# Kernel tuning notes

Measured on AMD Instinct MI355X. Metric: run time of the kernel, lower is better.

Reference implementation:

```python
import jax, jax.numpy as jnp
import numpy as np

L, D, H, V, T_BLK, B, T = 6, 768, 12, 32000, 1024, 4, 1024
HD = D // H          # head size = 64
FF = 4 * D           # FFN hidden
EPS = 1e-5


def _ln(x, g, b):
    m = x.mean(-1, keepdims=True)
    v = ((x - m) ** 2).mean(-1, keepdims=True)
    return (x - m) * jax.lax.rsqrt(v + EPS) * g + b


def _attn(q_in, kv_in, wqkv, wo, bo, causal):
    # wqkv: [3, D, D]; heads batched (equivalent to concat of per-head Linear outputs)
    Bq, Tq, _ = q_in.shape
    Tk = kv_in.shape[1]
    q = (q_in @ wqkv[0]).reshape(Bq, Tq, H, HD)
    k = (kv_in @ wqkv[1]).reshape(Bq, Tk, H, HD)
    v = (kv_in @ wqkv[2]).reshape(Bq, Tk, H, HD)
    wei = jnp.einsum('bqhd,bkhd->bhqk', q, k) * (HD ** -0.5)
    if causal:
        mask = jnp.tril(jnp.ones((Tq, Tk), dtype=bool))
        wei = jnp.where(mask, wei, -jnp.inf)
    wei = jax.nn.softmax(wei, axis=-1)
    out = jnp.einsum('bhqk,bkhd->bqhd', wei, v).reshape(Bq, Tq, D)
    return out @ wo + bo


def _ffn(x, w1, b1, w2, b2):
    return jax.nn.relu(x @ w1 + b1) @ w2 + b2


def _forward(idx, encoder_input,
             enc_tok, enc_pos, enc_qkv, enc_wo, enc_bo, enc_w1, enc_b1, enc_w2, enc_b2,
             enc_ln1g, enc_ln1b, enc_ln2g, enc_ln2b, enc_lnfg, enc_lnfb,
             dec_tok, dec_pos, dec_qkv, dec_wo, dec_bo, dec_cqkv, dec_cwo, dec_cbo,
             dec_w1, dec_b1, dec_w2, dec_b2,
             dec_ln1g, dec_ln1b, dec_ln2g, dec_ln2b, dec_ln3g, dec_ln3b,
             dec_lnfg, dec_lnfb, lm_w, lm_b):
    # ---- encoder (NOTE: original Head always applies causal tril, so encoder is causal) ----
    Te = encoder_input.shape[1]
    x = enc_tok[encoder_input] + enc_pos[:Te]
    for i in range(L):
        h = _ln(x, enc_ln1g[i], enc_ln1b[i])
        x = x + _attn(h, h, enc_qkv[i], enc_wo[i], enc_bo[i], causal=True)
        h = _ln(x, enc_ln2g[i], enc_ln2b[i])
        x = x + _ffn(h, enc_w1[i], enc_b1[i], enc_w2[i], enc_b2[i])
    enc_out = _ln(x, enc_lnfg, enc_lnfb)
    # ---- decoder ----
    Td = idx.shape[1]
    y = dec_tok[idx] + dec_pos[:Td]
    for i in range(L):
        h = _ln(y, dec_ln1g[i], dec_ln1b[i])
        y = y + _attn(h, h, dec_qkv[i], dec_wo[i], dec_bo[i], causal=True)
        h = _ln(y, dec_ln2g[i], dec_ln2b[i])
        y = y + _attn(h, enc_out, dec_cqkv[i], dec_cwo[i], dec_cbo[i], causal=False)
        h = _ln(y, dec_ln3g[i], dec_ln3b[i])
        y = y + _ffn(h, dec_w1[i], dec_b1[i], dec_w2[i], dec_b2[i])
    y = _ln(y, dec_lnfg, dec_lnfb)
    return y @ lm_w + lm_b  # logits [B, T, V]


def setup_inputs() -> dict:
    key = jax.random.key(0)
    keys = iter(jax.random.split(key, 80))
    def nrm(shape, s=0.02):
        return jax.random.normal(next(keys), shape, dtype=jnp.float32) * s
    z = lambda shape: jnp.zeros(shape, jnp.float32)
    o = lambda shape: jnp.ones(shape, jnp.float32)
    inp = {}
    inp['idx'] = jax.random.randint(next(keys), (B, T), 0, V)
    inp['encoder_input'] = jax.random.randint(next(keys), (B, T), 0, V)
    # encoder params
    inp['enc_tok'] = nrm((V, D)); inp['enc_pos'] = nrm((T_BLK, D))
    inp['enc_qkv'] = nrm((L, 3, D, D)); inp['enc_wo'] = nrm((L, D, D)); inp['enc_bo'] = z((L, D))
    inp['enc_w1'] = nrm((L, D, FF)); inp['enc_b1'] = z((L, FF))
    inp['enc_w2'] = nrm((L, FF, D)); inp['enc_b2'] = z((L, D))
    inp['enc_ln1g'] = o((L, D)); inp['enc_ln1b'] = z((L, D))
    inp['enc_ln2g'] = o((L, D)); inp['enc_ln2b'] = z((L, D))
    inp['enc_lnfg'] = o((D,)); inp['enc_lnfb'] = z((D,))
    # decoder params
    inp['dec_tok'] = nrm((V, D)); inp['dec_pos'] = nrm((T_BLK, D))
    inp['dec_qkv'] = nrm((L, 3, D, D)); inp['dec_wo'] = nrm((L, D, D)); inp['dec_bo'] = z((L, D))
    inp['dec_cqkv'] = nrm((L, 3, D, D)); inp['dec_cwo'] = nrm((L, D, D)); inp['dec_cbo'] = z((L, D))
    inp['dec_w1'] = nrm((L, D, FF)); inp['dec_b1'] = z((L, FF))
    inp['dec_w2'] = nrm((L, FF, D)); inp['dec_b2'] = z((L, D))
    inp['dec_ln1g'] = o((L, D)); inp['dec_ln1b'] = z((L, D))
    inp['dec_ln2g'] = o((L, D)); inp['dec_ln2b'] = z((L, D))
    inp['dec_ln3g'] = o((L, D)); inp['dec_ln3b'] = z((L, D))
    inp['dec_lnfg'] = o((D,)); inp['dec_lnfb'] = z((D,))
    inp['lm_w'] = nrm((D, V)); inp['lm_b'] = z((V,))
    return inp


def reference(idx, encoder_input,
              enc_tok, enc_pos, enc_qkv, enc_wo, enc_bo, enc_w1, enc_b1, enc_w2, enc_b2,
              enc_ln1g, enc_ln1b, enc_ln2g, enc_ln2b, enc_lnfg, enc_lnfb,
              dec_tok, dec_pos, dec_qkv, dec_wo, dec_bo, dec_cqkv, dec_cwo, dec_cbo,
              dec_w1, dec_b1, dec_w2, dec_b2,
              dec_ln1g, dec_ln1b, dec_ln2g, dec_ln2b, dec_ln3g, dec_ln3b,
              dec_lnfg, dec_lnfb, lm_w, lm_b):
    return _forward(idx, encoder_input,
                    enc_tok, enc_pos, enc_qkv, enc_wo, enc_bo, enc_w1, enc_b1, enc_w2, enc_b2,
                    enc_ln1g, enc_ln1b, enc_ln2g, enc_ln2b, enc_lnfg, enc_lnfb,
                    dec_tok, dec_pos, dec_qkv, dec_wo, dec_bo, dec_cqkv, dec_cwo, dec_cbo,
                    dec_w1, dec_b1, dec_w2, dec_b2,
                    dec_ln1g, dec_ln1b, dec_ln2g, dec_ln2b, dec_ln3g, dec_ln3b,
                    dec_lnfg, dec_lnfb, lm_w, lm_b)
```

## Files before the change

### kernel.cpp

```cpp
#include <hip/hip_runtime.h>


typedef __bf16 bf16x8 __attribute__((ext_vector_type(8)));
typedef float  f32x4  __attribute__((ext_vector_type(4)));
typedef unsigned short u16x4 __attribute__((ext_vector_type(4)));
typedef unsigned short u16x8 __attribute__((ext_vector_type(8)));

constexpr int Lc = 6, Dc = 768, Hc = 12, HDc = 64, Vc = 32000;
constexpr int Bc = 4, Tc = 1024, FFc = 3072;
constexpr int Mtot = Bc * Tc;

static __device__ __forceinline__ unsigned short f2bf(float f) {
  union { float f; unsigned u; } x; x.f = f;
  unsigned r = x.u + 0x7fffu + ((x.u >> 16) & 1u);
  return (unsigned short)(r >> 16);
}
static __device__ __forceinline__ float bf2f(unsigned short s) {
  union { unsigned u; float f; } c; c.u = (unsigned)s << 16; return c.f;
}

static __device__ __forceinline__ void gl_lds16(const unsigned short* g, unsigned short* l) {
  __builtin_amdgcn_global_load_lds(
      (const __attribute__((address_space(1))) unsigned int*)g,
      (__attribute__((address_space(3))) unsigned int*)l, 16, 0, 0);
}

static __device__ __forceinline__ float blockReduceSum(float v, float* red) {
  #pragma unroll
  for (int o = 32; o; o >>= 1) v += __shfl_xor(v, o, 64);
  int w = threadIdx.x >> 6;
  __syncthreads();
  if ((threadIdx.x & 63) == 0) red[w] = v;
  __syncthreads();
  return red[0] + red[1] + red[2] + red[3];
}

__global__ __launch_bounds__(256) void wconv_k(const float* __restrict__ W,
                                               unsigned short* __restrict__ WT,
                                               int K, int N) {
  __shared__ float t[32][33];
  const long zoff = (long)blockIdx.z * K * N;
  const int k0 = blockIdx.x * 32, n0 = blockIdx.y * 32;
  const int tid = threadIdx.x;
  const int rr = tid >> 3;
  const int cc = (tid & 7) * 4;
  f32x4 v = *reinterpret_cast<const f32x4*>(W + zoff + (long)(k0 + rr) * N + n0 + cc);
  #pragma unroll
  for (int j = 0; j < 4; j++) t[rr][cc + j] = v[j];
  __syncthreads();
  u16x4 o;
  #pragma unroll
  for (int j = 0; j < 4; j++) o[j] = f2bf(t[cc + j][rr]);
  *reinterpret_cast<u16x4*>(WT + zoff + (long)(n0 + rr) * K + k0 + cc) = o;
}

__global__ __launch_bounds__(256) void vtrans_k(const unsigned short* __restrict__ V,
                                                unsigned short* __restrict__ VT) {
  __shared__ unsigned short t[64][65];
  const int bh = blockIdx.y;
  const int b = bh / Hc, h = bh % Hc;
  const int t0 = blockIdx.x * 64;
  const int tid = threadIdx.x;
  const int rr = tid >> 3;
  const int c8 = (tid & 7) * 8;
  #pragma unroll
  for (int rep = 0; rep < 2; rep++) {
    int row = rep * 32 + rr;
    u16x8 v = *reinterpret_cast<const u16x8*>(V + (long)(b * Tc + t0 + row) * Dc + h * HDc + c8);
    #pragma unroll
    for (int j = 0; j < 8; j++) t[row][c8 + j] = v[j];
  }
  __syncthreads();
  #pragma unroll
  for (int rep = 0; rep < 2; rep++) {
    int hd = rep * 32 + rr;
    u16x8 o;
    #pragma unroll
    for (int j = 0; j < 8; j++) o[j] = t[c8 + j][hd];
    *reinterpret_cast<u16x8*>(VT + ((long)bh * HDc + hd) * Tc + t0 + c8) = o;
  }
}

__global__ __launch_bounds__(256) void embed_k(const int* __restrict__ idx,
                                               const float* __restrict__ tok,
                                               const float* __restrict__ pos,
                                               float* __restrict__ out) {
  const long row = blockIdx.x;
  const int t = (int)(row % Tc);
  const long id = idx[row];
  #pragma unroll
  for (int j = 0; j < 3; j++) {
    int e = threadIdx.x + j * 256;
    out[row * Dc + e] = tok[id * Dc + e] + pos[(long)t * Dc + e];
  }
}

__global__ __launch_bounds__(256) void ln_k(const float* __restrict__ X,
                                            const float* __restrict__ g,
                                            const float* __restrict__ bta,
                                            unsigned short* __restrict__ out) {
  __shared__ float red[4];
  const long row = blockIdx.x;
  const int tid = threadIdx.x;
  float v[3];
  #pragma unroll
  for (int j = 0; j < 3; j++) v[j] = X[row * Dc + tid + j * 256];
  float s = v[0] + v[1] + v[2];
  s = blockReduceSum(s, red);
  float mean = s * (1.f / 768.f);
  float q = 0.f;
  #pragma unroll
  for (int j = 0; j < 3; j++) { float d = v[j] - mean; q += d * d; }
  q = blockReduceSum(q, red);
  float rstd = rsqrtf(q * (1.f / 768.f) + 1e-5f);
  #pragma unroll
  for (int j = 0; j < 3; j++) {
    int e = tid + j * 256;
    out[row * Dc + e] = f2bf((v[j] - mean) * rstd * g[e] + bta[e]);
  }
}

template <bool CAUSAL>
__global__ __launch_bounds__(256) void flash_k(
    const unsigned short* __restrict__ Q,
    const unsigned short* __restrict__ K,
    const unsigned short* __restrict__ VT,
    unsigned short* __restrict__ O) {
  __shared__ __align__(16) unsigned short Ks[128 * 64];
  __shared__ __align__(16) unsigned short Vs[64 * 128];
  __shared__ __align__(16) unsigned short Ps[4][32 * 128];

  const int tid = threadIdx.x;
  const int lane = tid & 63;
  const int w = tid >> 6;
  const int lane16 = lane & 15;
  const int l4 = lane >> 4;
  const int bh = blockIdx.y;
  const int b = bh / Hc, h = bh % Hc;
  const int q0 = blockIdx.x * 128;

  const unsigned short* Qb = Q + ((long)b * Tc) * Dc + h * HDc;
  const unsigned short* Kb = K + ((long)b * Tc) * Dc + h * HDc;
  const unsigned short* Vb = VT + (long)bh * HDc * Tc;
  unsigned short* Ob = O + ((long)b * Tc) * Dc + h * HDc;

  bf16x8 qf[2][2];
  #pragma unroll
  for (int m = 0; m < 2; m++)
    #pragma unroll
    for (int kk = 0; kk < 2; kk++) {
      u16x8 raw = *reinterpret_cast<const u16x8*>(
          Qb + (long)(q0 + w * 32 + m * 16 + lane16) * Dc + kk * 32 + l4 * 8);
      bf16x8 f;
      #pragma unroll
      for (int j = 0; j < 8; j++) f[j] = (__bf16)(bf2f(raw[j]) * 0.125f);
      qf[m][kk] = f;
    }

  float mrow[2][4], lrow[2][4];
  f32x4 accO[2][4];
  #pragma unroll
  for (int m = 0; m < 2; m++)
    #pragma unroll
    for (int r = 0; r < 4; r++) { mrow[m][r] = -1e30f; lrow[m][r] = 0.f; }
  #pragma unroll
  for (int m = 0; m < 2; m++)
    #pragma unroll
    for (int d4 = 0; d4 < 4; d4++)
      #pragma unroll
      for (int r = 0; r < 4; r++) accO[m][d4][r] = 0.f;

  const int nch = CAUSAL ? (blockIdx.x + 1) : (Tc / 128);
  for (int c = 0; c < nch; c++) {
    const int k0 = c * 128;
    __syncthreads();
    #pragma unroll
    for (int it = 0; it < 4; it++) {
      int u = (it * 4 + w) * 64 + lane;
      int r = u >> 3, s = u & 7;
      gl_lds16(Kb + (long)(k0 + r) * Dc + ((s ^ (r & 7)) * 8), &Ks[(it * 4 + w) * 512]);
      int r2 = u >> 4, s2 = u & 15;
      gl_lds16(Vb + (long)r2 * Tc + k0 + ((s2 ^ (r2 & 7)) * 8), &Vs[(it * 4 + w) * 512]);
    }
    __syncthreads();

    f32x4 sacc[2][8];
    #pragma unroll
    for (int m = 0; m < 2; m++)
      #pragma unroll
      for (int n = 0; n < 8; n++)
        #pragma unroll
        for (int r = 0; r < 4; r++) sacc[m][n][r] = 0.f;
    #pragma unroll
    for (int n = 0; n < 8; n++) {
      int row = n * 16 + lane16;
      #pragma unroll
      for (int kk = 0; kk < 2; kk++) {
        bf16x8 kf = *reinterpret_cast<const bf16x8*>(
            &Ks[row * 64 + (((kk * 4 + l4) ^ (row & 7)) * 8)]);
        sacc[0][n] = __builtin_amdgcn_mfma_f32_16x16x32_bf16(qf[0][kk], kf, sacc[0][n], 0, 0, 0);
        sacc[1][n] = __builtin_amdgcn_mfma_f32_16x16x32_bf16(qf[1][kk], kf, sacc[1][n], 0, 0, 0);
      }
    }

    if (CAUSAL && c == nch - 1) {
      #pragma unroll
      for (int m = 0; m < 2; m++)
        #pragma unroll
        for (int n = 0; n < 8; n++)
          #pragma unroll
          for (int r = 0; r < 4; r++) {
            int kcol = k0 + n * 16 + lane16;
            int q = q0 + w * 32 + m * 16 + l4 * 4 + r;
            if (kcol > q) sacc[m][n][r] = -1e30f;
          }
    }

    #pragma unroll
    for (int m = 0; m < 2; m++)
      #pragma unroll
      for (int r = 0; r < 4; r++) {
        float smax = sacc[m][0][r];
        #pragma unroll
        for (int n = 1; n < 8; n++) smax = fmaxf(smax, sacc[m][n][r]);
        #pragma unroll
        for (int off = 1; off < 16; off <<= 1) smax = fmaxf(smax, __shfl_xor(smax, off, 64));
        float mold = mrow[m][r];
        float mnew = fmaxf(mold, smax);
        float sc = __expf(mold - mnew);
        float psum = 0.f;
        unsigned short pv[8];
        #pragma unroll
        for (int n = 0; n < 8; n++) {
          float p = __expf(sacc[m][n][r] - mnew);
          psum += p;
          pv[n] = f2bf(p);
        }
        #pragma unroll
        for (int off = 1; off < 16; off <<= 1) psum += __shfl_xor(psum, off, 64);
        lrow[m][r] = lrow[m][r] * sc + psum;
        mrow[m][r] = mnew;
        #pragma unroll
        for (int d4 = 0; d4 < 4; d4++) accO[m][d4][r] *= sc;
        int prow = m * 16 + l4 * 4 + r;
        #pragma unroll
        for (int n = 0; n < 8; n++) {
          int col = n * 16 + lane16;
          Ps[w][prow * 128 + (((col >> 3) ^ (prow & 7)) * 8) + (col & 7)] = pv[n];
        }
      }

    #pragma unroll
    for (int kk = 0; kk < 4; kk++) {
      bf16x8 pa[2];
      #pragma unroll
      for (int m = 0; m < 2; m++) {
        int arow = m * 16 + lane16;
        pa[m] = *reinterpret_cast<const bf16x8*>(
            &Ps[w][arow * 128 + (((kk * 4 + l4) ^ (arow & 7)) * 8)]);
      }
      #pragma unroll
      for (int d4 = 0; d4 < 4; d4++) {
        int vrow = d4 * 16 + lane16;
        bf16x8 vf = *reinterpret_cast<const bf16x8*>(
            &Vs[vrow * 128 + (((kk * 4 + l4) ^ (vrow & 7)) * 8)]);
        accO[0][d4] = __builtin_amdgcn_mfma_f32_16x16x32_bf16(pa[0], vf, accO[0][d4], 0, 0, 0);
        accO[1][d4] = __builtin_amdgcn_mfma_f32_16x16x32_bf16(pa[1], vf, accO[1][d4], 0, 0, 0);
      }
    }
  }

  #pragma unroll
  for (int m = 0; m < 2; m++)
    #pragma unroll
    for (int r = 0; r < 4; r++) {
      float inv = 1.f / lrow[m][r];
      int q = q0 + w * 32 + m * 16 + l4 * 4 + r;
      #pragma unroll
      for (int d4 = 0; d4 < 4; d4++)
        Ob[(long)q * Dc + d4 * 16 + lane16] = f2bf(accO[m][d4][r] * inv);
    }
}

template <int BM, int BN, int MF, int NF, bool HASBIAS, bool RELU, bool HASRES, bool OUTBF>
__global__ __launch_bounds__(256) void gemm_k(
    const unsigned short* __restrict__ A, long sAb, long sAh, int lda,
    const unsigned short* __restrict__ BT, long sBb, long sBh, int ldb,
    void* Cp, long sCb, long sCh, int ldc,
    const float* __restrict__ bias,
    const float* __restrict__ Res, int ldr,
    int K, int nH, float alpha) {
  constexpr int BK = 64;
  __shared__ __align__(16) unsigned short As[2][BM * BK];
  __shared__ __align__(16) unsigned short Bs[2][BN * BK];

  const int tid = threadIdx.x;
  const int lane = tid & 63;
  const int w = tid >> 6;
  const int wr = w >> 1, wc = w & 1;
  const int lane16 = lane & 15;
  const int l4 = lane >> 4;

  const int z = blockIdx.z;
  const int bb = z / nH, hh = z % nH;
  const long offA = sAb * bb + sAh * hh;
  const long offB = sBb * bb + sBh * hh;
  const long offC = sCb * bb + sCh * hh;

  const int m0 = blockIdx.x * BM;
  const int n0 = blockIdx.y * BN;

  const int sr = lane >> 3;
  const int sgl = ((lane & 7) ^ sr) * 8;

  const unsigned short* Ab = A + offA + (long)m0 * lda;
  const unsigned short* Bb = BT + offB + (long)n0 * ldb;

  const unsigned short* aP[BM / 32];
  #pragma unroll
  for (int j = 0; j < BM / 32; j++)
    aP[j] = Ab + (long)(w * (BM / 4) + j * 8 + sr) * lda + sgl;
  const unsigned short* bP[BN / 32];
  #pragma unroll
  for (int j = 0; j < BN / 32; j++)
    bP[j] = Bb + (long)(w * (BN / 4) + j * 8 + sr) * ldb + sgl;

  f32x4 acc[MF][NF];
  #pragma unroll
  for (int m = 0; m < MF; m++)
    #pragma unroll
    for (int n = 0; n < NF; n++)
      #pragma unroll
      for (int r = 0; r < 4; r++) acc[m][n][r] = 0.f;

  auto STAGE = [&](int buf, int k0) {
    #pragma unroll
    for (int j = 0; j < BM / 32; j++)
      gl_lds16(aP[j] + k0, &As[buf][(w * (BM / 4) + j * 8) * BK]);
    #pragma unroll
    for (int j = 0; j < BN / 32; j++)
      gl_lds16(bP[j] + k0, &Bs[buf][(w * (BN / 4) + j * 8) * BK]);
  };
  auto COMPUTE = [&](int buf) {
    #pragma unroll
    for (int kk = 0; kk < 2; kk++) {
      bf16x8 af[MF], bfr[NF];
      #pragma unroll
      for (int m = 0; m < MF; m++) {
        int row = wr * MF * 16 + m * 16 + lane16;
        af[m] = *reinterpret_cast<const bf16x8*>(
            &As[buf][row * BK + (((kk * 4 + l4) ^ (lane16 & 7)) * 8)]);
      }
      #pragma unroll
      for (int n = 0; n < NF; n++) {
        int row = wc * NF * 16 + n * 16 + lane16;
        bfr[n] = *reinterpret_cast<const bf16x8*>(
            &Bs[buf][row * BK + (((kk * 4 + l4) ^ (lane16 & 7)) * 8)]);
      }
      #pragma unroll
      for (int m = 0; m < MF; m++)
        #pragma unroll
        for (int n = 0; n < NF; n++)
          acc[m][n] = __builtin_amdgcn_mfma_f32_16x16x32_bf16(af[m], bfr[n], acc[m][n], 0, 0, 0);
    }
  };

  const int nt = K / BK;
  int cur = 0;
  STAGE(0, 0);
  __syncthreads();
  for (int t = 0; t < nt; t++) {
    if (t + 1 < nt) STAGE(cur ^ 1, (t + 1) * BK);
    COMPUTE(cur);
    __syncthreads();
    cur ^= 1;
  }

  const int r0 = m0 + wr * MF * 16;
  const int c0 = n0 + wc * NF * 16;
  #pragma unroll
  for (int m = 0; m < MF; m++) {
    #pragma unroll
    for (int n = 0; n < NF; n++) {
      #pragma unroll
      for (int r = 0; r < 4; r++) {
        int rr = r0 + m * 16 + l4 * 4 + r;
        int cc = c0 + n * 16 + lane16;
        float v = acc[m][n][r] * alpha;
        if constexpr (HASBIAS) v += bias[cc];
        if constexpr (RELU) v = fmaxf(v, 0.f);
        if constexpr (HASRES) v += Res[offC + (long)rr * ldr + cc];
        if constexpr (OUTBF) ((unsigned short*)Cp)[offC + (long)rr * ldc + cc] = f2bf(v);
        else                 ((float*)Cp)[offC + (long)rr * ldc + cc] = v;
      }
    }
  }
}

extern "C" void kernel_launch(void* const* d_in, const int* in_sizes, int n_in,
                              void* d_out, int out_size, void* d_ws, size_t ws_size,
                              hipStream_t stream) {
  (void)in_sizes; (void)n_in; (void)out_size;

  const int*   idx      = (const int*)d_in[0];
  const int*   enc_in   = (const int*)d_in[1];
  const float* enc_tok  = (const float*)d_in[2];
  const float* enc_pos  = (const float*)d_in[3];
  const float* enc_qkv  = (const float*)d_in[4];
  const float* enc_wo   = (const float*)d_in[5];
  const float* enc_bo   = (const float*)d_in[6];
  const float* enc_w1   = (const float*)d_in[7];
  const float* enc_b1   = (const float*)d_in[8];
  const float* enc_w2   = (const float*)d_in[9];
  const float* enc_b2   = (const float*)d_in[10];
  const float* enc_ln1g = (const float*)d_in[11];
  const float* enc_ln1b = (const float*)d_in[12];
  const float* enc_ln2g = (const float*)d_in[13];
  const float* enc_ln2b = (const float*)d_in[14];
  const float* enc_lnfg = (const float*)d_in[15];
  const float* enc_lnfb = (const float*)d_in[16];
  const float* dec_tok  = (const float*)d_in[17];
  const float* dec_pos  = (const float*)d_in[18];
  const float* dec_qkv  = (const float*)d_in[19];
  const float* dec_wo   = (const float*)d_in[20];
  const float* dec_bo   = (const float*)d_in[21];
  const float* dec_cqkv = (const float*)d_in[22];
  const float* dec_cwo  = (const float*)d_in[23];
  const float* dec_cbo  = (const float*)d_in[24];
  const float* dec_w1   = (const float*)d_in[25];
  const float* dec_b1   = (const float*)d_in[26];
  const float* dec_w2   = (const float*)d_in[27];
  const float* dec_b2   = (const float*)d_in[28];
  const float* dec_ln1g = (const float*)d_in[29];
  const float* dec_ln1b = (const float*)d_in[30];
  const float* dec_ln2g = (const float*)d_in[31];
  const float* dec_ln2b = (const float*)d_in[32];
  const float* dec_ln3g = (const float*)d_in[33];
  const float* dec_ln3b = (const float*)d_in[34];
  const float* dec_lnfg = (const float*)d_in[35];
  const float* dec_lnfb = (const float*)d_in[36];
  const float* lm_w     = (const float*)d_in[37];
  const float* lm_b     = (const float*)d_in[38];

  constexpr long De2 = (long)Dc * Dc;
  constexpr long DF  = (long)Dc * FFc;

  unsigned short* wcache = (unsigned short*)d_out;
  size_t woff = 0;
  auto take = [&](size_t n) { unsigned short* p = wcache + woff; woff += n; return p; };
  unsigned short* enc_qkvT  = take(18ul * De2);
  unsigned short* enc_woT   = take(6ul * De2);
  unsigned short* enc_w1T   = take(6ul * DF);
  unsigned short* enc_w2T   = take(6ul * DF);
  unsigned short* dec_qkvT  = take(18ul * De2);
  unsigned short* dec_woT   = take(6ul * De2);
  unsigned short* dec_cqkvT = take(18ul * De2);
  unsigned short* dec_cwoT  = take(6ul * De2);
  unsigned short* dec_w1T   = take(6ul * DF);
  unsigned short* dec_w2T   = take(6ul * DF);

  char* ws = (char*)d_ws;
  const size_t need = (size_t)Dc * Vc * 2 + 2ull * Mtot * Dc * 4 + 3ull * Mtot * Dc * 2 +
                      3ull * Mtot * Dc * 2 + (size_t)Mtot * FFc * 2 + (size_t)Mtot * Dc * 2 +
                      (size_t)Bc * Hc * HDc * Tc * 2 + 4096;
  if (ws_size < need) return;
  auto takeW = [&](size_t bytes) { char* p = ws; ws += (bytes + 255) & ~255ull; return p; };
  unsigned short* lm_wT = (unsigned short*)takeW((size_t)Dc * Vc * 2);
  float* xe             = (float*)takeW((size_t)Mtot * Dc * 4);
  float* xd             = (float*)takeW((size_t)Mtot * Dc * 4);
  unsigned short* hbf   = (unsigned short*)takeW((size_t)Mtot * Dc * 2);
  unsigned short* qkvb  = (unsigned short*)takeW(3ull * Mtot * Dc * 2);
  unsigned short* ao    = (unsigned short*)takeW((size_t)Mtot * Dc * 2);
  unsigned short* mid   = (unsigned short*)takeW((size_t)Mtot * FFc * 2);
  unsigned short* eo    = (unsigned short*)takeW((size_t)Mtot * Dc * 2);
  unsigned short* vT    = (unsigned short*)takeW((size_t)Bc * Hc * HDc * Tc * 2);
  unsigned short* qb = qkvb;
  unsigned short* kb = qkvb + (size_t)Mtot * Dc;
  unsigned short* vb = qkvb + 2ull * Mtot * Dc;

  const dim3 TB(256);

  wconv_k<<<dim3(Dc/32, Dc/32, 18), TB, 0, stream>>>(enc_qkv, enc_qkvT, Dc, Dc);
  wconv_k<<<dim3(Dc/32, Dc/32,  6), TB, 0, stream>>>(enc_wo,  enc_woT,  Dc, Dc);
  wconv_k<<<dim3(Dc/32, FFc/32, 6), TB, 0, stream>>>(enc_w1,  enc_w1T,  Dc, FFc);
  wconv_k<<<dim3(FFc/32, Dc/32, 6), TB, 0, stream>>>(enc_w2,  enc_w2T,  FFc, Dc);
  wconv_k<<<dim3(Dc/32, Dc/32, 18), TB, 0, stream>>>(dec_qkv, dec_qkvT, Dc, Dc);
  wconv_k<<<dim3(Dc/32, Dc/32,  6), TB, 0, stream>>>(dec_wo,  dec_woT,  Dc, Dc);
  wconv_k<<<dim3(Dc/32, Dc/32, 18), TB, 0, stream>>>(dec_cqkv,dec_cqkvT,Dc, Dc);
  wconv_k<<<dim3(Dc/32, Dc/32,  6), TB, 0, stream>>>(dec_cwo, dec_cwoT, Dc, Dc);
  wconv_k<<<dim3(Dc/32, FFc/32, 6), TB, 0, stream>>>(dec_w1,  dec_w1T,  Dc, FFc);
  wconv_k<<<dim3(FFc/32, Dc/32, 6), TB, 0, stream>>>(dec_w2,  dec_w2T,  FFc, Dc);
  wconv_k<<<dim3(Dc/32, Vc/32,  1), TB, 0, stream>>>(lm_w,    lm_wT,    Dc, Vc);

  auto LN = [&](const float* X, const float* g, const float* b, unsigned short* o) {
    ln_k<<<dim3(Mtot), TB, 0, stream>>>(X, g, b, o);
  };
  auto QKV3 = [&](const unsigned short* Abf, const unsigned short* W3T) {
    gemm_k<128,64,4,2,false,false,false,true><<<dim3(Mtot/128, Dc/64, 3), TB, 0, stream>>>(
        Abf, 0, 0, Dc, W3T, De2, 0, Dc,
        qkvb, (long)Mtot*Dc, 0, Dc, nullptr, nullptr, 0, Dc, 1, 1.f);
  };
  auto PROJ1 = [&](const unsigned short* Abf, const unsigned short* WT, unsigned short* Cb) {
    gemm_k<128,64,4,2,false,false,false,true><<<dim3(Mtot/128, Dc/64, 1), TB, 0, stream>>>(
        Abf, 0, 0, Dc, WT, 0, 0, Dc,
        Cb, 0, 0, Dc, nullptr, nullptr, 0, Dc, 1, 1.f);
  };
  auto KV2 = [&](const unsigned short* Abf, const unsigned short* W2T) {
    gemm_k<128,64,4,2,false,false,false,true><<<dim3(Mtot/128, Dc/64, 2), TB, 0, stream>>>(
        Abf, 0, 0, Dc, W2T, De2, 0, Dc,
        kb, (long)Mtot*Dc, 0, Dc, nullptr, nullptr, 0, Dc, 1, 1.f);
  };
  auto VT = [&]() {
    vtrans_k<<<dim3(Tc/64, Bc*Hc), TB, 0, stream>>>(vb, vT);
  };
  auto FLASH = [&](bool causal) {
    if (causal) flash_k<true ><<<dim3(Tc/128, Bc*Hc), TB, 0, stream>>>(qb, kb, vT, ao);
    else        flash_k<false><<<dim3(Tc/128, Bc*Hc), TB, 0, stream>>>(qb, kb, vT, ao);
  };
  auto ORES = [&](const unsigned short* Abf, const unsigned short* WT, const float* bias, float* X) {
    gemm_k<128,64,4,2,true,false,true,false><<<dim3(Mtot/128, Dc/64, 1), TB, 0, stream>>>(
        Abf, 0, 0, Dc, WT, 0, 0, Dc,
        X, 0, 0, Dc, bias, X, Dc, Dc, 1, 1.f);
  };
  auto FFN1 = [&](const unsigned short* Abf, const unsigned short* WT, const float* bias) {
    gemm_k<128,128,4,4,true,true,false,true><<<dim3(Mtot/128, FFc/128, 1), TB, 0, stream>>>(
        Abf, 0, 0, Dc, WT, 0, 0, Dc,
        mid, 0, 0, FFc, bias, nullptr, 0, Dc, 1, 1.f);
  };
  auto FFN2 = [&](const unsigned short* WT, const float* bias, float* X) {
    gemm_k<128,64,4,2,true,false,true,false><<<dim3(Mtot/128, Dc/64, 1), TB, 0, stream>>>(
        mid, 0, 0, FFc, WT, 0, 0, FFc,
        X, 0, 0, Dc, bias, X, Dc, FFc, 1, 1.f);
  };

  embed_k<<<dim3(Mtot), TB, 0, stream>>>(enc_in, enc_tok, enc_pos, xe);
  for (int i = 0; i < Lc; i++) {
    LN(xe, enc_ln1g + i * Dc, enc_ln1b + i * Dc, hbf);
    QKV3(hbf, enc_qkvT + (size_t)i * 3 * De2);
    VT(); FLASH(true);
    ORES(ao, enc_woT + (size_t)i * De2, enc_bo + i * Dc, xe);
    LN(xe, enc_ln2g + i * Dc, enc_ln2b + i * Dc, hbf);
    FFN1(hbf, enc_w1T + (size_t)i * DF, enc_b1 + i * FFc);
    FFN2(enc_w2T + (size_t)i * DF, enc_b2 + i * Dc, xe);
  }
  LN(xe, enc_lnfg, enc_lnfb, eo);

  embed_k<<<dim3(Mtot), TB, 0, stream>>>(idx, dec_tok, dec_pos, xd);
  for (int i = 0; i < Lc; i++) {
    LN(xd, dec_ln1g + i * Dc, dec_ln1b + i * Dc, hbf);
    QKV3(hbf, dec_qkvT + (size_t)i * 3 * De2);
    VT(); FLASH(true);
    ORES(ao, dec_woT + (size_t)i * De2, dec_bo + i * Dc, xd);
    LN(xd, dec_ln2g + i * Dc, dec_ln2b + i * Dc, hbf);
    PROJ1(hbf, dec_cqkvT + (size_t)i * 3 * De2, qb);
    KV2(eo, dec_cqkvT + (size_t)i * 3 * De2 + De2);
    VT(); FLASH(false);
    ORES(ao, dec_cwoT + (size_t)i * De2, dec_cbo + i * Dc, xd);
    LN(xd, dec_ln3g + i * Dc, dec_ln3b + i * Dc, hbf);
    FFN1(hbf, dec_w1T + (size_t)i * DF, dec_b1 + i * FFc);
    FFN2(dec_w2T + (size_t)i * DF, dec_b2 + i * Dc, xd);
  }
  LN(xd, dec_lnfg, dec_lnfb, hbf);

  gemm_k<128,128,4,4,true,false,false,false><<<dim3(Mtot/128, Vc/128, 1), TB, 0, stream>>>(
      hbf, 0, 0, Dc, lm_wT, 0, 0, Dc,
      d_out, 0, 0, Vc, lm_b, nullptr, 0, Dc, 1, 1.f);
}
```

Baseline: 3.936 ms.

## Add 256x256-tile triple-buffered GEMM for QKV, FFN1 and LM head

Adds a new GEMM kernel with 512-thread blocks computing 256x256 output tiles. It uses a 3-stage global-to-LDS pipeline with BK=32, swizzled LDS reads, and an XCD-aware block remapping to improve L2 locality. The kernel replaces the 128x64 and 128x128 GEMMs for the QKV projection, the first FFN layer and the large LM-head projection, aiming for more data reuse per tile. In exchange, the small QKV and FFN1 grids leave many CUs idle. The 128 accumulators per thread plus fragments under launch_bounds(512,2) risk register pressure or spills.

```diff
diff --git a/kernel.cpp b/kernel.cpp
--- a/kernel.cpp
+++ b/kernel.cpp
@@ -280,6 +280,127 @@
       for (int d4 = 0; d4 < 4; d4++)
         Ob[(long)q * Dc + d4 * 16 + lane16] = f2bf(accO[m][d4][r] * inv);
     }
+}
+
+template <bool HASBIAS, bool RELU, bool OUTBF>
+__global__ __launch_bounds__(512, 2) void gemm256_k(
+    const unsigned short* __restrict__ A, long sAz, int lda,
+    const unsigned short* __restrict__ BT, long sBz, int ldb,
+    void* Cp, long sCz, int ldc,
+    const float* __restrict__ bias, int K) {
+  __shared__ __align__(16) unsigned short As[3][256 * 32];
+  __shared__ __align__(16) unsigned short Bs[3][256 * 32];
+
+  const int tid = threadIdx.x;
+  const int lane = tid & 63;
+  const int w = tid >> 6;
+  const int lane16 = lane & 15;
+  const int l4 = lane >> 4;
+  const int wrM = (w >> 2) * 128;
+  const int wcN = (w & 3) * 64;
+
+  const int nwg = gridDim.x * gridDim.y;
+  const int id = blockIdx.y * gridDim.x + blockIdx.x;
+  const int q8 = nwg >> 3, r8 = nwg & 7;
+  const int xcd = id & 7, ord = id >> 3;
+  const int swz = (xcd < r8 ? xcd * (q8 + 1) : r8 * (q8 + 1) + (xcd - r8) * q8) + ord;
+  const int m0 = (swz % gridDim.x) * 256;
+  const int n0 = (swz / gridDim.x) * 256;
+
+  const long offA = sAz * blockIdx.z;
+  const long offB = sBz * blockIdx.z;
+  const long offC = sCz * blockIdx.z;
+
+  const int srow = lane >> 2;
+  const int sslot = ((lane & 3) ^ ((srow >> 1) & 3)) * 8;
+
+  const unsigned short* aP[2];
+  const unsigned short* bP[2];
+  #pragma unroll
+  for (int j = 0; j < 2; j++) {
+    int rb = w * 32 + j * 16;
+    aP[j] = A + offA + (long)(m0 + rb + srow) * lda + sslot;
+    bP[j] = BT + offB + (long)(n0 + rb + srow) * ldb + sslot;
+  }
+
+  f32x4 acc[8][4];
+  #pragma unroll
+  for (int m = 0; m < 8; m++)
+    #pragma unroll
+    for (int n = 0; n < 4; n++)
+      #pragma unroll
+      for (int r = 0; r < 4; r++) acc[m][n][r] = 0.f;
+
+  auto STAGE = [&](int buf, int k0) {
+    #pragma unroll
+    for (int j = 0; j < 2; j++) {
+      gl_lds16(aP[j] + k0, &As[buf][(w * 32 + j * 16) * 32]);
+      gl_lds16(bP[j] + k0, &Bs[buf][(w * 32 + j * 16) * 32]);
+    }
+  };
+
+  const int nt = K / 32;
+  STAGE(0, 0);
+  STAGE(1, 32);
+  int cur = 0, nx2 = 2;
+  for (int t = 0; t < nt; t++) {
+    if (t + 2 < nt) {
+      STAGE(nx2, (t + 2) * 32);
+      asm volatile("s_waitcnt vmcnt(8)" ::: "memory");
+    } else if (t + 1 < nt) {
+      asm volatile("s_waitcnt vmcnt(4)" ::: "memory");
+    } else {
+      asm volatile("s_waitcnt vmcnt(0)" ::: "memory");
+    }
+    __builtin_amdgcn_sched_barrier(0);
+    __builtin_amdgcn_s_barrier();
+    __builtin_amdgcn_sched_barrier(0);
+
+    bf16x8 afr[8], bfr[4];
+    #pragma unroll
+    for (int n = 0; n < 4; n++) {
+      int row = wcN + n * 16 + lane16;
+      bfr[n] = *reinterpret_cast<const bf16x8*>(
+          &Bs[cur][row * 32 + ((l4 ^ ((row >> 1) & 3)) * 8)]);
+    }
+    #pragma unroll
+    for (int m = 0; m < 8; m++) {
+      int row = wrM + m * 16 + lane16;
+      afr[m] = *reinterpret_cast<const bf16x8*>(
+          &As[cur][row * 32 + ((l4 ^ ((row >> 1) & 3)) * 8)]);
+    }
+    __builtin_amdgcn_s_setprio(1);
+    #pragma unroll
+    for (int m = 0; m < 8; m++)
+      #pragma unroll
+      for (int n = 0; n < 4; n++)
+        acc[m][n] = __builtin_amdgcn_mfma_f32_16x16x32_bf16(afr[m], bfr[n], acc[m][n], 0, 0, 0);
+    __builtin_amdgcn_s_setprio(0);
+
+    asm volatile("s_waitcnt lgkmcnt(0)" ::: "memory");
+    __builtin_amdgcn_sched_barrier(0);
+    __builtin_amdgcn_s_barrier();
+    __builtin_amdgcn_sched_barrier(0);
+    cur = (cur == 2) ? 0 : cur + 1;
+    nx2 = (nx2 == 2) ? 0 : nx2 + 1;
+  }
+
+  #pragma unroll
+  for (int m = 0; m < 8; m++) {
+    #pragma unroll
+    for (int n = 0; n < 4; n++) {
+      #pragma unroll
+      for (int r = 0; r < 4; r++) {
+        int rr = m0 + wrM + m * 16 + l4 * 4 + r;
+        int cc = n0 + wcN + n * 16 + lane16;
+        float v = acc[m][n][r];
+        if constexpr (HASBIAS) v += bias[cc];
+        if constexpr (RELU) v = fmaxf(v, 0.f);
+        if constexpr (OUTBF) ((unsigned short*)Cp)[offC + (long)rr * ldc + cc] = f2bf(v);
+        else                 ((float*)Cp)[offC + (long)rr * ldc + cc] = v;
+      }
+    }
+  }
 }
 
 template <int BM, int BN, int MF, int NF, bool HASBIAS, bool RELU, bool HASRES, bool OUTBF>
@@ -496,9 +617,8 @@
     ln_k<<<dim3(Mtot), TB, 0, stream>>>(X, g, b, o);
   };
   auto QKV3 = [&](const unsigned short* Abf, const unsigned short* W3T) {
-    gemm_k<128,64,4,2,false,false,false,true><<<dim3(Mtot/128, Dc/64, 3), TB, 0, stream>>>(
-        Abf, 0, 0, Dc, W3T, De2, 0, Dc,
-        qkvb, (long)Mtot*Dc, 0, Dc, nullptr, nullptr, 0, Dc, 1, 1.f);
+    gemm256_k<false,false,true><<<dim3(Mtot/256, Dc/256, 3), dim3(512), 0, stream>>>(
+        Abf, 0, Dc, W3T, De2, Dc, qkvb, (long)Mtot*Dc, Dc, nullptr, Dc);
   };
   auto PROJ1 = [&](const unsigned short* Abf, const unsigned short* WT, unsigned short* Cb) {
     gemm_k<128,64,4,2,false,false,false,true><<<dim3(Mtot/128, Dc/64, 1), TB, 0, stream>>>(
@@ -523,9 +643,8 @@
         X, 0, 0, Dc, bias, X, Dc, Dc, 1, 1.f);
   };
   auto FFN1 = [&](const unsigned short* Abf, const unsigned short* WT, const float* bias) {
-    gemm_k<128,128,4,4,true,true,false,true><<<dim3(Mtot/128, FFc/128, 1), TB, 0, stream>>>(
-        Abf, 0, 0, Dc, WT, 0, 0, Dc,
-        mid, 0, 0, FFc, bias, nullptr, 0, Dc, 1, 1.f);
+    gemm256_k<true,true,true><<<dim3(Mtot/256, FFc/256, 1), dim3(512), 0, stream>>>(
+        Abf, 0, Dc, WT, 0, Dc, mid, 0, FFc, bias, Dc);
   };
   auto FFN2 = [&](const unsigned short* WT, const float* bias, float* X) {
     gemm_k<128,64,4,2,true,false,true,false><<<dim3(Mtot/128, Dc/64, 1), TB, 0, stream>>>(
@@ -562,7 +681,6 @@
   }
   LN(xd, dec_lnfg, dec_lnfb, hbf);
 
-  gemm_k<128,128,4,4,true,false,false,false><<<dim3(Mtot/128, Vc/128, 1), TB, 0, stream>>>(
-      hbf, 0, 0, Dc, lm_wT, 0, 0, Dc,
-      d_out, 0, 0, Vc, lm_b, nullptr, 0, Dc, 1, 1.f);
-}
+  gemm256_k<true,false,false><<<dim3(Mtot/256, Vc/256, 1), dim3(512), 0, stream>>>(
+      hbf, 0, Dc, lm_wT, 0, Dc, d_out, 0, Vc, lm_b, Dc);
+}
```

New measurement: 4.018 ms. 2.1% more time.

## Restructure GEMM main loop with BK=32, explicit waitcnt, XCD swizzle, occupancy hints

Applied to the files above, without the earlier changes.

The GEMM kernel now uses BK=32 K-tiles with a new LDS swizzle and a manual double-buffer pipeline. It issues the next stage's global-to-LDS loads, then waits on vmcnt and uses raw s_barrier with sched_barrier fences, and raises priority around the MFMA block. Workgroup ids are remapped so blocks that share data land on the same XCD, and launch_bounds gain a min-waves hint. The QKV projection switches to 128x128 tiles. These aim to cut synchronisation overhead, improve L2 locality and raise occupancy. The cost is more barriers per K-step and a correctness dependence on the hand-written waitcnt counts.

```diff
diff --git a/kernel.cpp b/kernel.cpp
--- a/kernel.cpp
+++ b/kernel.cpp
@@ -23,6 +23,12 @@
   __builtin_amdgcn_global_load_lds(
       (const __attribute__((address_space(1))) unsigned int*)g,
       (__attribute__((address_space(3))) unsigned int*)l, 16, 0, 0);
+}
+
+template <int N> static __device__ __forceinline__ void wait_vm() {
+  if constexpr (N == 0)      asm volatile("s_waitcnt vmcnt(0)" ::: "memory");
+  else if constexpr (N == 3) asm volatile("s_waitcnt vmcnt(3)" ::: "memory");
+  else if constexpr (N == 4) asm volatile("s_waitcnt vmcnt(4)" ::: "memory");
 }
 
 static __device__ __forceinline__ float blockReduceSum(float v, float* red) {
@@ -282,17 +288,20 @@
     }
 }
 
-template <int BM, int BN, int MF, int NF, bool HASBIAS, bool RELU, bool HASRES, bool OUTBF>
-__global__ __launch_bounds__(256) void gemm_k(
+template <int BM, int BN, int MF, int NF, int MINW,
+          bool HASBIAS, bool RELU, bool HASRES, bool OUTBF>
+__global__ __launch_bounds__(256, MINW) void gemm_k(
     const unsigned short* __restrict__ A, long sAb, long sAh, int lda,
     const unsigned short* __restrict__ BT, long sBb, long sBh, int ldb,
     void* Cp, long sCb, long sCh, int ldc,
     const float* __restrict__ bias,
     const float* __restrict__ Res, int ldr,
     int K, int nH, float alpha) {
-  constexpr int BK = 64;
-  __shared__ __align__(16) unsigned short As[2][BM * BK];
-  __shared__ __align__(16) unsigned short Bs[2][BN * BK];
+  constexpr int AI = BM / 64;
+  constexpr int BI = BN / 64;
+  constexpr int VC = AI + BI;
+  __shared__ __align__(16) unsigned short As[2][BM * 32];
+  __shared__ __align__(16) unsigned short Bs[2][BN * 32];
 
   const int tid = threadIdx.x;
   const int lane = tid & 63;
@@ -307,23 +316,26 @@
   const long offB = sBb * bb + sBh * hh;
   const long offC = sCb * bb + sCh * hh;
 
-  const int m0 = blockIdx.x * BM;
-  const int n0 = blockIdx.y * BN;
-
-  const int sr = lane >> 3;
-  const int sgl = ((lane & 7) ^ sr) * 8;
-
-  const unsigned short* Ab = A + offA + (long)m0 * lda;
-  const unsigned short* Bb = BT + offB + (long)n0 * ldb;
-
-  const unsigned short* aP[BM / 32];
-  #pragma unroll
-  for (int j = 0; j < BM / 32; j++)
-    aP[j] = Ab + (long)(w * (BM / 4) + j * 8 + sr) * lda + sgl;
-  const unsigned short* bP[BN / 32];
-  #pragma unroll
-  for (int j = 0; j < BN / 32; j++)
-    bP[j] = Bb + (long)(w * (BN / 4) + j * 8 + sr) * ldb + sgl;
+  const int gx = gridDim.x;
+  const int nwg = gx * gridDim.y;
+  const int id = blockIdx.y * gx + blockIdx.x;
+  const int q8 = nwg >> 3, r8 = nwg & 7;
+  const int xcd = id & 7, ord = id >> 3;
+  const int swz = (xcd < r8 ? xcd * (q8 + 1) : r8 * (q8 + 1) + (xcd - r8) * q8) + ord;
+  const int m0 = (swz % gx) * BM;
+  const int n0 = (swz / gx) * BN;
+
+  const int srow = lane >> 2;
+  const int sslot = ((lane & 3) ^ ((srow >> 1) & 3)) * 8;
+
+  const unsigned short* aP[AI];
+  #pragma unroll
+  for (int j = 0; j < AI; j++)
+    aP[j] = A + offA + (long)(m0 + w * (BM / 4) + j * 16 + srow) * lda + sslot;
+  const unsigned short* bP[BI];
+  #pragma unroll
+  for (int j = 0; j < BI; j++)
+    bP[j] = BT + offB + (long)(n0 + w * (BN / 4) + j * 16 + srow) * ldb + sslot;
 
   f32x4 acc[MF][NF];
   #pragma unroll
@@ -335,44 +347,47 @@
 
   auto STAGE = [&](int buf, int k0) {
     #pragma unroll
-    for (int j = 0; j < BM / 32; j++)
-      gl_lds16(aP[j] + k0, &As[buf][(w * (BM / 4) + j * 8) * BK]);
-    #pragma unroll
-    for (int j = 0; j < BN / 32; j++)
-      gl_lds16(bP[j] + k0, &Bs[buf][(w * (BN / 4) + j * 8) * BK]);
-  };
-  auto COMPUTE = [&](int buf) {
-    #pragma unroll
-    for (int kk = 0; kk < 2; kk++) {
-      bf16x8 af[MF], bfr[NF];
-      #pragma unroll
-      for (int m = 0; m < MF; m++) {
-        int row = wr * MF * 16 + m * 16 + lane16;
-        af[m] = *reinterpret_cast<const bf16x8*>(
-            &As[buf][row * BK + (((kk * 4 + l4) ^ (lane16 & 7)) * 8)]);
-      }
-      #pragma unroll
-      for (int n = 0; n < NF; n++) {
-        int row = wc * NF * 16 + n * 16 + lane16;
-        bfr[n] = *reinterpret_cast<const bf16x8*>(
-            &Bs[buf][row * BK + (((kk * 4 + l4) ^ (lane16 & 7)) * 8)]);
-      }
-      #pragma unroll
-      for (int m = 0; m < MF; m++)
-        #pragma unroll
-        for (int n = 0; n < NF; n++)
-          acc[m][n] = __builtin_amdgcn_mfma_f32_16x16x32_bf16(af[m], bfr[n], acc[m][n], 0, 0, 0);
-    }
-  };
-
-  const int nt = K / BK;
+    for (int j = 0; j < AI; j++)
+      gl_lds16(aP[j] + k0, &As[buf][(w * (BM / 4) + j * 16) * 32]);
+    #pragma unroll
+    for (int j = 0; j < BI; j++)
+      gl_lds16(bP[j] + k0, &Bs[buf][(w * (BN / 4) + j * 16) * 32]);
+  };
+
+  const int nt = K / 32;
+  STAGE(0, 0);
   int cur = 0;
-  STAGE(0, 0);
-  __syncthreads();
   for (int t = 0; t < nt; t++) {
-    if (t + 1 < nt) STAGE(cur ^ 1, (t + 1) * BK);
-    COMPUTE(cur);
-    __syncthreads();
+    if (t + 1 < nt) { STAGE(cur ^ 1, (t + 1) * 32); wait_vm<VC>(); }
+    else            { wait_vm<0>(); }
+    __builtin_amdgcn_sched_barrier(0);
+    __builtin_amdgcn_s_barrier();
+    __builtin_amdgcn_sched_barrier(0);
+
+    bf16x8 afr[MF], bfr[NF];
+    #pragma unroll
+    for (int n = 0; n < NF; n++) {
+      int row = wc * NF * 16 + n * 16 + lane16;
+      bfr[n] = *reinterpret_cast<const bf16x8*>(
+          &Bs[cur][row * 32 + ((l4 ^ ((row >> 1) & 3)) * 8)]);
+    }
+    #pragma unroll
+    for (int m = 0; m < MF; m++) {
+      int row = wr * MF * 16 + m * 16 + lane16;
+      afr[m] = *reinterpret_cast<const bf16x8*>(
+          &As[cur][row * 32 + ((l4 ^ ((row >> 1) & 3)) * 8)]);
+    }
+    __builtin_amdgcn_s_setprio(1);
+    #pragma unroll
+    for (int m = 0; m < MF; m++)
+      #pragma unroll
+      for (int n = 0; n < NF; n++)
+        acc[m][n] = __builtin_amdgcn_mfma_f32_16x16x32_bf16(afr[m], bfr[n], acc[m][n], 0, 0, 0);
+    __builtin_amdgcn_s_setprio(0);
+
+    asm volatile("s_waitcnt lgkmcnt(0)" ::: "memory");
+    __builtin_amdgcn_sched_barrier(0);
+    __builtin_amdgcn_s_barrier();
     cur ^= 1;
   }
 
@@ -496,17 +511,17 @@
     ln_k<<<dim3(Mtot), TB, 0, stream>>>(X, g, b, o);
   };
   auto QKV3 = [&](const unsigned short* Abf, const unsigned short* W3T) {
-    gemm_k<128,64,4,2,false,false,false,true><<<dim3(Mtot/128, Dc/64, 3), TB, 0, stream>>>(
+    gemm_k<128,128,4,4,3,false,false,false,true><<<dim3(Mtot/128, Dc/128, 3), TB, 0, stream>>>(
         Abf, 0, 0, Dc, W3T, De2, 0, Dc,
         qkvb, (long)Mtot*Dc, 0, Dc, nullptr, nullptr, 0, Dc, 1, 1.f);
   };
   auto PROJ1 = [&](const unsigned short* Abf, const unsigned short* WT, unsigned short* Cb) {
-    gemm_k<128,64,4,2,false,false,false,true><<<dim3(Mtot/128, Dc/64, 1), TB, 0, stream>>>(
+    gemm_k<128,64,4,2,4,false,false,false,true><<<dim3(Mtot/128, Dc/64, 1), TB, 0, stream>>>(
         Abf, 0, 0, Dc, WT, 0, 0, Dc,
         Cb, 0, 0, Dc, nullptr, nullptr, 0, Dc, 1, 1.f);
   };
   auto KV2 = [&](const unsigned short* Abf, const unsigned short* W2T) {
-    gemm_k<128,64,4,2,false,false,false,true><<<dim3(Mtot/128, Dc/64, 2), TB, 0, stream>>>(
+    gemm_k<128,64,4,2,4,false,false,false,true><<<dim3(Mtot/128, Dc/64, 2), TB, 0, stream>>>(
         Abf, 0, 0, Dc, W2T, De2, 0, Dc,
         kb, (long)Mtot*Dc, 0, Dc, nullptr, nullptr, 0, Dc, 1, 1.f);
   };
@@ -518,17 +533,17 @@
     else        flash_k<false><<<dim3(Tc/128, Bc*Hc), TB, 0, stream>>>(qb, kb, vT, ao);
   };
   auto ORES = [&](const unsigned short* Abf, const unsigned short* WT, const float* bias, float* X) {
-    gemm_k<128,64,4,2,true,false,true,false><<<dim3(Mtot/128, Dc/64, 1), TB, 0, stream>>>(
+    gemm_k<128,64,4,2,4,true,false,true,false><<<dim3(Mtot/128, Dc/64, 1), TB, 0, stream>>>(
         Abf, 0, 0, Dc, WT, 0, 0, Dc,
         X, 0, 0, Dc, bias, X, Dc, Dc, 1, 1.f);
   };
   auto FFN1 = [&](const unsigned short* Abf, const unsigned short* WT, const float* bias) {
-    gemm_k<128,128,4,4,true,true,false,true><<<dim3(Mtot/128, FFc/128, 1), TB, 0, stream>>>(
+    gemm_k<128,128,4,4,3,true,true,false,true><<<dim3(Mtot/128, FFc/128, 1), TB, 0, stream>>>(
         Abf, 0, 0, Dc, WT, 0, 0, Dc,
         mid, 0, 0, FFc, bias, nullptr, 0, Dc, 1, 1.f);
   };
   auto FFN2 = [&](const unsigned short* WT, const float* bias, float* X) {
-    gemm_k<128,64,4,2,true,false,true,false><<<dim3(Mtot/128, Dc/64, 1), TB, 0, stream>>>(
+    gemm_k<128,64,4,2,4,true,false,true,false><<<dim3(Mtot/128, Dc/64, 1), TB, 0, stream>>>(
         mid, 0, 0, FFc, WT, 0, 0, FFc,
         X, 0, 0, Dc, bias, X, Dc, FFc, 1, 1.f);
   };
@@ -562,7 +577,7 @@
   }
   LN(xd, dec_lnfg, dec_lnfb, hbf);
 
-  gemm_k<128,128,4,4,true,false,false,false><<<dim3(Mtot/128, Vc/128, 1), TB, 0, stream>>>(
+  gemm_k<128,128,4,4,3,true,false,false,false><<<dim3(Mtot/128, Vc/128, 1), TB, 0, stream>>>(
       hbf, 0, 0, Dc, lm_wT, 0, 0, Dc,
       d_out, 0, 0, Vc, lm_b, nullptr, 0, Dc, 1, 1.f);
 }
```

Result: slower. 4.025 ms (+2.3%).
